# Optimization experiments

Measured on AMD Instinct MI355X. Metric: run time of the kernel, lower is better.

Reference implementation:

```python
import jax, jax.numpy as jnp
import numpy as np

NDIGIT = 10
DIM_IN = 256
DIM_OUT = 784
BATCH = 16384


def setup_inputs() -> dict:
    key = jax.random.key(0)
    k_theta, k_label, k_W = jax.random.split(key, 3)
    theta = jax.random.normal(k_theta, (BATCH, DIM_IN), dtype=jnp.float32)
    label = jax.random.randint(k_label, (BATCH,), 0, NDIGIT, dtype=jnp.int32)
    # xavier_uniform for each (dim_out, dim_in) matrix
    limit = float(np.sqrt(6.0 / (DIM_IN + DIM_OUT)))
    megaW = jax.random.uniform(k_W, (NDIGIT, DIM_OUT, DIM_IN), dtype=jnp.float32,
                               minval=-limit, maxval=limit)
    megab = jnp.zeros((NDIGIT, DIM_OUT), dtype=jnp.float32)
    return {"theta": theta, "label": label, "megaW": megaW, "megab": megab}


def reference(theta, label, megaW, megab):
    # Dense compute across all 10 digit experts (matches torch.bmm over repeated theta)
    # added: [b, ndigit, dim_out]
    added = jnp.einsum('ndi,bi->bnd', megaW, theta) + megab[None, :, :]
    # Select the expert output per example by label (vector_gather)
    selected = jnp.take_along_axis(added, label[:, None, None].astype(jnp.int32), axis=1)[:, 0, :]
    probs = jax.nn.sigmoid(selected)
    return probs
```

## Files before the change

### kernel.cpp

```cpp
#include <hip/hip_runtime.h>
#include <hip/hip_bf16.h>

#define NDIGIT 10
#define DIM_IN 256
#define DIM_OUT 784
#define BATCH 16384
#define NCT 49
#define TM 16
#define MAX_T16 (BATCH / TM + NDIGIT)
#define RBS 788

#define WS_IDX 1024
#define WS_DESC 17408
#define WS_WBF_BYTES 81920
#define WS_TH_BYTES (WS_WBF_BYTES + 2007040 * 2)

typedef __attribute__((ext_vector_type(4))) float f32x4;
typedef __attribute__((ext_vector_type(8))) short bf16x8;

__device__ __forceinline__ short f2bf(float f) {
    union { float f; unsigned u; } c; c.f = f;
    unsigned u = c.u;
    u += 0x7fffu + ((u >> 16) & 1u);
    return (short)(u >> 16);
}

__global__ void prep_k(const float* __restrict__ megaW,
                       const int* __restrict__ label,
                       int* __restrict__ wsi,
                       short* __restrict__ wbf) {
    int b = blockIdx.x, t = threadIdx.x;
    if (b < 980) {
        int idx = b * 256 + t;
        int gi = idx >> 9;
        int ks = (idx >> 6) & 7;
        int l  = idx & 63;
        int g  = gi / 49;
        int ct = gi - g * 49;
        int col = ct * 16 + (l & 15);
        int k   = ks * 32 + ((l >> 4) << 3);
        const float* src = megaW + ((size_t)(g * DIM_OUT + col) * DIM_IN + k);
        f32x4 v0 = *(const f32x4*)src;
        f32x4 v1 = *(const f32x4*)(src + 4);
        bf16x8 o;
        o[0] = f2bf(v0[0]); o[1] = f2bf(v0[1]); o[2] = f2bf(v0[2]); o[3] = f2bf(v0[3]);
        o[4] = f2bf(v1[0]); o[5] = f2bf(v1[1]); o[6] = f2bf(v1[2]); o[7] = f2bf(v1[3]);
        *(bf16x8*)(wbf + (size_t)idx * 8) = o;
    } else {
        __shared__ int h[NDIGIT];
        int j = b - 980;
        if (t < NDIGIT) h[t] = 0;
        __syncthreads();
        int i0 = j * 512;
        atomicAdd(&h[label[i0 + t]], 1);
        atomicAdd(&h[label[i0 + 256 + t]], 1);
        __syncthreads();
        if (t < NDIGIT) wsi[64 + j * 16 + t] = h[t];
    }
}

__global__ void scatter2_k(const int* __restrict__ label, int* __restrict__ wsi) {
    __shared__ int tot[NDIGIT], bef[NDIGIT], base[NDIGIT + 1], cur[NDIGIT], toff[NDIGIT + 1];
    int j = blockIdx.x, t = threadIdx.x;
    if (t < NDIGIT) {
        int s = 0, sb = 0;
        for (int jj = 0; jj < 32; ++jj) {
            int v = wsi[64 + jj * 16 + t];
            s += v;
            if (jj < j) sb += v;
        }
        tot[t] = s; bef[t] = sb;
    }
    __syncthreads();
    if (t == 0) {
        int off = 0, tf = 0;
        for (int g = 0; g < NDIGIT; ++g) {
            base[g] = off; toff[g] = tf;
            off += tot[g]; tf += (tot[g] + TM - 1) / TM;
        }
        base[NDIGIT] = off; toff[NDIGIT] = tf;
    }
    __syncthreads();
    if (t < NDIGIT) cur[t] = base[t] + bef[t];
    if (j == 0) {
        int ptotal = toff[NDIGIT];
        for (int p = t; p < ptotal; p += 512) {
            int g2 = 0;
            while (p >= toff[g2 + 1]) ++g2;
            int row0 = (p - toff[g2]) * TM;
            int rcv = tot[g2] - row0; if (rcv > TM) rcv = TM;
            wsi[WS_DESC + p] = (base[g2] + row0) | (rcv << 14) | (g2 << 21);
        }
        if (t < NDIGIT) wsi[t] = base[t];
        if (t == 0) { wsi[10] = base[NDIGIT]; wsi[24] = ptotal; }
    }
    __syncthreads();
    int i = j * 512 + t;
    int g = label[i];
    int r = atomicAdd(&cur[g], 1);
    wsi[WS_IDX + r] = i;
}

__global__ void gth_k(const float* __restrict__ theta,
                      const int* __restrict__ wsi,
                      short* __restrict__ thsort) {
    int gid = blockIdx.x * 256 + threadIdx.x;
    int r = gid >> 5;
    int c8 = (gid & 31) << 3;
    int src = wsi[WS_IDX + r];
    const float* p = theta + (size_t)src * DIM_IN + c8;
    f32x4 v0 = *(const f32x4*)p;
    f32x4 v1 = *(const f32x4*)(p + 4);
    bf16x8 o;
    o[0] = f2bf(v0[0]); o[1] = f2bf(v0[1]); o[2] = f2bf(v0[2]); o[3] = f2bf(v0[3]);
    o[4] = f2bf(v1[0]); o[5] = f2bf(v1[1]); o[6] = f2bf(v1[2]); o[7] = f2bf(v1[3]);
    *(bf16x8*)(thsort + (size_t)r * DIM_IN + c8) = o;
}


#define LOADB(B, CT) do {                                                      \
    const short* Bt_ = Wg + (size_t)(CT) * 4096 + l * 8;                       \
    _Pragma("unroll")                                                          \
    for (int ks = 0; ks < 8; ++ks)                                             \
        (B)[ks] = *(const bf16x8*)(Bt_ + ks * 512);                            \
} while (0)

#define TILE13(B, CT) do {                                                     \
    float bias_ = bgb[(CT) * 16 + r16];                                        \
    f32x4 acc_ = {0.f, 0.f, 0.f, 0.f};                                         \
    _Pragma("unroll")                                                          \
    for (int ks = 0; ks < 8; ++ks)                                             \
        acc_ = __builtin_amdgcn_mfma_f32_16x16x32_bf16(a[ks], (B)[ks], acc_, 0, 0, 0); \
    _Pragma("unroll")                                                          \
    for (int j = 0; j < 4; ++j) {                                              \
        float x_ = acc_[j] + bias_;                                            \
        rowbuf[(kg * 4 + j) * RBS + (CT) * 16 + r16] = 1.0f / (1.0f + __expf(-x_)); \
    }                                                                          \
} while (0)

__launch_bounds__(256, 3)
__global__ void moe_gemm13_k(const short* __restrict__ thsort,
                             const float* __restrict__ megab,
                             const int* __restrict__ wsi,
                             const short* __restrict__ wbf,
                             float* __restrict__ out) {
    __shared__ float rowbuf[TM * RBS];

    int Bid = blockIdx.x;
    const int q8 = MAX_T16 / 8, r8 = MAX_T16 % 8;
    int xcd = Bid & 7, slot = Bid >> 3;
    int p = (xcd < r8 ? xcd * (q8 + 1) : r8 * (q8 + 1) + (xcd - r8) * q8) + slot;

    int total = wsi[24];
    if (p >= total) return;

    int d = wsi[WS_DESC + p];
    int startRow = d & 0x3FFF;
    int rc = (d >> 14) & 0x7F;
    int g  = d >> 21;

    int tid = threadIdx.x;
    int wv = tid >> 6, l = tid & 63, r16 = l & 15, kg = l >> 4;

    int mloc = r16; if (mloc >= rc) mloc = rc - 1;
    const short* Ar = thsort + (size_t)(startRow + mloc) * DIM_IN + kg * 8;
    bf16x8 a[8];
#pragma unroll
    for (int ks = 0; ks < 8; ++ks)
        a[ks] = *(const bf16x8*)(Ar + ks * 32);

    const short* Wg  = wbf + (size_t)g * (NCT * 4096);
    const float* bgb = megab + (size_t)g * DIM_OUT;

    bf16x8 bA[8], bB[8];
    int ct = wv;
    LOADB(bA, ct);
    while (true) {
        int c1 = ct + 4;
        if (c1 < NCT) { LOADB(bB, c1); TILE13(bA, ct); }
        else          { TILE13(bA, ct); break; }
        int c2 = c1 + 4;
        if (c2 < NCT) { LOADB(bA, c2); TILE13(bB, c1); }
        else          { TILE13(bB, c1); break; }
        ct = c2;
    }

    __syncthreads();

    const int* idxl = wsi + WS_IDX + startRow;
#pragma unroll
    for (int s = 0; s < 13; ++s) {
        int c = s * 256 + tid;
        if (c < TM * 196) {
            int row = c / 196;
            int cir = c - row * 196;
            if (row < rc) {
                f32x4 v = *(const f32x4*)(rowbuf + row * RBS + cir * 4);
                *(f32x4*)(out + (size_t)idxl[row] * DIM_OUT + cir * 4) = v;
            }
        }
    }
}

extern "C" void kernel_launch(void* const* d_in, const int* in_sizes, int n_in,
                              void* d_out, int out_size, void* d_ws, size_t ws_size,
                              hipStream_t stream) {
    const float* theta = (const float*)d_in[0];
    const int*   label = (const int*)d_in[1];
    const float* megaW = (const float*)d_in[2];
    const float* megab = (const float*)d_in[3];
    float* out = (float*)d_out;
    int* wsi = (int*)d_ws;
    short* wbf    = (short*)((char*)d_ws + WS_WBF_BYTES);
    short* thsort = (short*)((char*)d_ws + WS_TH_BYTES);

    prep_k     <<<1012, 256, 0, stream>>>(megaW, label, wsi, wbf);
    scatter2_k <<<32, 512, 0, stream>>>(label, wsi);
    gth_k      <<<2048, 256, 0, stream>>>(theta, wsi, thsort);
    moe_gemm13_k<<<MAX_T16, 256, 0, stream>>>(thsort, megab, wsi, wbf, out);
}
```

Measured before the change: 49.80 us.

## Use 512-thread GEMM blocks with bf16 shared staging and no B double-buffer

The grouped GEMM kernel now runs 8 waves per block instead of 4, each covering column tiles with stride 8. The explicit B-register double buffering is dropped in favour of a simple loop that relies on more resident waves to hide latency. The sigmoid results are staged in shared memory as bf16 rather than fp32, which halves LDS use and allows higher occupancy. Outputs are widened back to fp32 on store, so there is an added precision loss in the output from bf16 rounding of the probabilities.

Measured after the change: 53.38 us. 7.2% more time.

```diff
diff --git a/kernel.cpp b/kernel.cpp
--- a/kernel.cpp
+++ b/kernel.cpp
@@ -8,7 +8,7 @@
 #define NCT 49
 #define TM 16
 #define MAX_T16 (BATCH / TM + NDIGIT)
-#define RBS 788
+#define RBSS 792
 
 #define WS_IDX 1024
 #define WS_DESC 17408
@@ -17,6 +17,7 @@
 
 typedef __attribute__((ext_vector_type(4))) float f32x4;
 typedef __attribute__((ext_vector_type(8))) short bf16x8;
+typedef __attribute__((ext_vector_type(4))) unsigned short u16x4;
 
 __device__ __forceinline__ short f2bf(float f) {
     union { float f; unsigned u; } c; c.f = f;
@@ -117,34 +118,13 @@
     *(bf16x8*)(thsort + (size_t)r * DIM_IN + c8) = o;
 }
 
-
-#define LOADB(B, CT) do {                                                      \
-    const short* Bt_ = Wg + (size_t)(CT) * 4096 + l * 8;                       \
-    _Pragma("unroll")                                                          \
-    for (int ks = 0; ks < 8; ++ks)                                             \
-        (B)[ks] = *(const bf16x8*)(Bt_ + ks * 512);                            \
-} while (0)
-
-#define TILE13(B, CT) do {                                                     \
-    float bias_ = bgb[(CT) * 16 + r16];                                        \
-    f32x4 acc_ = {0.f, 0.f, 0.f, 0.f};                                         \
-    _Pragma("unroll")                                                          \
-    for (int ks = 0; ks < 8; ++ks)                                             \
-        acc_ = __builtin_amdgcn_mfma_f32_16x16x32_bf16(a[ks], (B)[ks], acc_, 0, 0, 0); \
-    _Pragma("unroll")                                                          \
-    for (int j = 0; j < 4; ++j) {                                              \
-        float x_ = acc_[j] + bias_;                                            \
-        rowbuf[(kg * 4 + j) * RBS + (CT) * 16 + r16] = 1.0f / (1.0f + __expf(-x_)); \
-    }                                                                          \
-} while (0)
-
-__launch_bounds__(256, 3)
-__global__ void moe_gemm13_k(const short* __restrict__ thsort,
+__launch_bounds__(512, 6)
+__global__ void moe_gemm14_k(const short* __restrict__ thsort,
                              const float* __restrict__ megab,
                              const int* __restrict__ wsi,
                              const short* __restrict__ wbf,
                              float* __restrict__ out) {
-    __shared__ float rowbuf[TM * RBS];
+    __shared__ short rowbuf[TM * RBSS];
 
     int Bid = blockIdx.x;
     const int q8 = MAX_T16 / 8, r8 = MAX_T16 % 8;
@@ -172,31 +152,45 @@
     const short* Wg  = wbf + (size_t)g * (NCT * 4096);
     const float* bgb = megab + (size_t)g * DIM_OUT;
 
-    bf16x8 bA[8], bB[8];
-    int ct = wv;
-    LOADB(bA, ct);
-    while (true) {
-        int c1 = ct + 4;
-        if (c1 < NCT) { LOADB(bB, c1); TILE13(bA, ct); }
-        else          { TILE13(bA, ct); break; }
-        int c2 = c1 + 4;
-        if (c2 < NCT) { LOADB(bA, c2); TILE13(bB, c1); }
-        else          { TILE13(bB, c1); break; }
-        ct = c2;
+    for (int ct = wv; ct < NCT; ct += 8) {
+        const short* Bt = Wg + (size_t)ct * 4096 + l * 8;
+        bf16x8 b[8];
+#pragma unroll
+        for (int ks = 0; ks < 8; ++ks)
+            b[ks] = *(const bf16x8*)(Bt + ks * 512);
+
+        f32x4 acc = {0.f, 0.f, 0.f, 0.f};
+#pragma unroll
+        for (int ks = 0; ks < 8; ++ks)
+            acc = __builtin_amdgcn_mfma_f32_16x16x32_bf16(a[ks], b[ks], acc, 0, 0, 0);
+
+        float bias = bgb[ct * 16 + r16];
+#pragma unroll
+        for (int j = 0; j < 4; ++j) {
+            float x = acc[j] + bias;
+            float pv = 1.0f / (1.0f + __expf(-x));
+            rowbuf[(kg * 4 + j) * RBSS + ct * 16 + r16] = f2bf(pv);
+        }
     }
 
     __syncthreads();
 
     const int* idxl = wsi + WS_IDX + startRow;
 #pragma unroll
-    for (int s = 0; s < 13; ++s) {
-        int c = s * 256 + tid;
+    for (int s = 0; s < 7; ++s) {
+        int c = s * 512 + tid;
         if (c < TM * 196) {
             int row = c / 196;
             int cir = c - row * 196;
             if (row < rc) {
-                f32x4 v = *(const f32x4*)(rowbuf + row * RBS + cir * 4);
-                *(f32x4*)(out + (size_t)idxl[row] * DIM_OUT + cir * 4) = v;
+                u16x4 v = *(const u16x4*)(rowbuf + row * RBSS + cir * 4);
+                union { unsigned u; float f; } c0, c1, c2, c3;
+                c0.u = (unsigned)v[0] << 16;
+                c1.u = (unsigned)v[1] << 16;
+                c2.u = (unsigned)v[2] << 16;
+                c3.u = (unsigned)v[3] << 16;
+                f32x4 o = { c0.f, c1.f, c2.f, c3.f };
+                *(f32x4*)(out + (size_t)idxl[row] * DIM_OUT + cir * 4) = o;
             }
         }
     }
@@ -214,8 +208,8 @@
     short* wbf    = (short*)((char*)d_ws + WS_WBF_BYTES);
     short* thsort = (short*)((char*)d_ws + WS_TH_BYTES);
 
-    prep_k     <<<1012, 256, 0, stream>>>(megaW, label, wsi, wbf);
-    scatter2_k <<<32, 512, 0, stream>>>(label, wsi);
-    gth_k      <<<2048, 256, 0, stream>>>(theta, wsi, thsort);
-    moe_gemm13_k<<<MAX_T16, 256, 0, stream>>>(thsort, megab, wsi, wbf, out);
-}
+    prep_k      <<<1012, 256, 0, stream>>>(megaW, label, wsi, wbf);
+    scatter2_k  <<<32, 512, 0, stream>>>(label, wsi);
+    gth_k       <<<2048, 256, 0, stream>>>(theta, wsi, thsort);
+    moe_gemm14_k<<<MAX_T16, 512, 0, stream>>>(thsort, megab, wsi, wbf, out);
+}
```
